# Kernel optimization log

Hardware: AMD Instinct MI355X
Metric: run time of the kernel (lower is better)

## Reference

```python
import jax, jax.numpy as jnp
import numpy as np

N_NODES = 16384
N_EDGES = 131072
MUL = 64                # multiplicity of 0e and 1o node irreps
N_RADIAL = 8
HIDDEN = 64
NUM_IRREPS = 6 * MUL    # 192x0e + 192x1o after concat/regroup
AVG_NUM_NEIGHBORS = 8.0
INV_SQRT3 = 1.0 / np.sqrt(3.0)  # wigner-3j(1,1,0) component normalization


def setup_inputs() -> dict:
    key = jax.random.key(0)
    ks = jax.random.split(key, 8)
    return {
        "node_feats": jax.random.normal(ks[0], (N_NODES, MUL + 3 * MUL), jnp.float32),
        "edge_features": jax.random.normal(ks[1], (N_EDGES, 4), jnp.float32),
        "radial_embedding": jax.random.uniform(ks[2], (N_EDGES, N_RADIAL), jnp.float32),
        "w1": jax.random.normal(ks[3], (N_RADIAL, HIDDEN), jnp.float32),
        "w2": jax.random.normal(ks[4], (HIDDEN, HIDDEN), jnp.float32),
        "w3": jax.random.normal(ks[5], (HIDDEN, NUM_IRREPS), jnp.float32),
        "senders": jax.random.randint(ks[6], (N_EDGES,), 0, N_NODES),
        "receivers": jax.random.randint(ks[7], (N_EDGES,), 0, N_NODES),
    }


def reference(node_feats, edge_features, radial_embedding, w1, w2, w3, senders, receivers):
    N = node_feats.shape[0]
    E = senders.shape[0]
    # split node irreps: 64x0e (scalars) + 64x1o (vectors)
    s = node_feats[:, :MUL]                       # [N, 64]
    v = node_feats[:, MUL:].reshape(N, MUL, 3)    # [N, 64, 3]
    # gather by sender
    s_e = s[senders]                              # [E, 64]
    v_e = v[senders]                              # [E, 64, 3]
    # edge attrs: 1x0e + 1x1o (spherical harmonics l<=1)
    es = edge_features[:, :1]                     # [E, 1]
    ev = edge_features[:, 1:4]                    # [E, 3]
    # CG tensor product filtered to {0e, 1o} (component normalization)
    tp_s1 = s_e * es                                              # 0e x 0e -> 0e
    tp_s2 = jnp.einsum("emc,ec->em", v_e, ev) * INV_SQRT3        # 1o x 1o -> 0e
    tp_v1 = s_e[:, :, None] * ev[:, None, :]                      # 0e x 1o -> 1o
    tp_v2 = v_e * es[:, :, None]                                  # 1o x 0e -> 1o
    # concat(filtered node feats, tp output) regrouped -> 192x0e + 192x1o
    scal = jnp.concatenate([s_e, tp_s1, tp_s2], axis=1)          # [E, 192]
    vec = jnp.concatenate([v_e, tp_v1, tp_v2], axis=1)           # [E, 192, 3]
    # radial MLP (no bias, e3nn 1/sqrt(fan_in) scaling, no output activation)
    h = jax.nn.silu(radial_embedding @ w1 / np.sqrt(N_RADIAL))
    h = jax.nn.silu(h @ w2 / np.sqrt(HIDDEN))
    w = h @ w3 / np.sqrt(HIDDEN)                                  # [E, 384]
    n_scal = scal.shape[1]
    scal = scal * w[:, :n_scal]
    vec = vec * w[:, n_scal:, None]
    # scatter-add into receivers
    out_s = jnp.zeros((N, n_scal), scal.dtype).at[receivers].add(scal)
    out_v = jnp.zeros((N, n_scal, 3), vec.dtype).at[receivers].add(vec)
    out = jnp.concatenate([out_s, out_v.reshape(N, n_scal * 3)], axis=1)
    return out / np.sqrt(AVG_NUM_NEIGHBORS)
```

## Files before the change

kernel.cpp:

```cpp
#include <hip/hip_runtime.h>

#define N_NODES 16384
#define N_EDGES 131072
#define MUL 64
#define HIDDEN 64
#define NUM_IRREPS 384
#define TE 64

#define INV_SQRT3   0.5773502691896258f
#define INV_SQRT8   0.35355339059327373f
#define SC3         (0.125f * 0.35355339059327373f)

typedef __attribute__((ext_vector_type(8))) __bf16 bf16x8;
typedef __attribute__((ext_vector_type(8))) unsigned short ushort8;
typedef __attribute__((ext_vector_type(4))) float f32x4;

union FragU { ushort8 u; bf16x8 b; };

__device__ __forceinline__ float silu_f(float x) {
    return x / (1.0f + __expf(-x));
}
__device__ __forceinline__ unsigned short bf16_rn(float f) {
    union { float f; unsigned int u; } c; c.f = f;
    unsigned int u = c.u + 0x7FFFu + ((c.u >> 16) & 1u);
    return (unsigned short)(u >> 16);
}
__device__ __forceinline__ float bf16_to_f(unsigned short h) {
    union { unsigned int u; float f; } c; c.u = ((unsigned int)h) << 16;
    return c.f;
}

__global__ __launch_bounds__(256) void pack_kernel(
    const float* __restrict__ w2, const float* __restrict__ w3,
    unsigned short* __restrict__ w2p, unsigned short* __restrict__ w3p)
{
    int t = blockIdx.x * 256 + threadIdx.x;
    float v;
    unsigned short *hi_dst, *lo_dst;
    if (t < 4096) {
        int K = t >> 11, T = (t >> 9) & 3, lane = (t >> 3) & 63, j = t & 7;
        int k = K * 32 + (lane >> 4) * 8 + j;
        int n = T * 16 + (lane & 15);
        v = w2[k * 64 + n] * 0.125f;
        hi_dst = w2p + t; lo_dst = w2p + 4096 + t;
    } else if (t < 28672) {
        int u = t - 4096;
        int K = u / 12288; int rem = u - K * 12288;
        int T = rem >> 9, lane = (rem >> 3) & 63, j = rem & 7;
        int k = K * 32 + (lane >> 4) * 8 + j;
        int n = T * 16 + (lane & 15);
        v = w3[k * 384 + n] * SC3;
        hi_dst = w3p + u; lo_dst = w3p + 24576 + u;
    } else {
        return;
    }
    unsigned short h = bf16_rn(v);
    unsigned short l = bf16_rn(v - bf16_to_f(h));
    *hi_dst = h; *lo_dst = l;
}

__global__ __launch_bounds__(256) void mlp_kernel(
    const float* __restrict__ radial,
    const float* __restrict__ w1,
    const unsigned short* __restrict__ w2p,
    const unsigned short* __restrict__ w3p,
    float* __restrict__ wout,
    int e_begin)
{
    __shared__ float w1s[512];
    __shared__ float rs[64 * 9];
    __shared__ float h1s[64 * 68];
    __shared__ float h2s[64 * 68];

    const int t   = threadIdx.x;
    const int le0 = blockIdx.x * TE;
    const int e0  = e_begin + le0;

    for (int i = t; i < 512; i += 256) w1s[i] = w1[i];
    for (int i = t; i < 512; i += 256)
        rs[(i >> 3) * 9 + (i & 7)] = radial[(size_t)e0 * 8 + i];
    __syncthreads();

    {
        const int e  = t >> 2;
        const int j0 = (t & 3) * 16;
        float acc[16];
#pragma unroll
        for (int j = 0; j < 16; ++j) acc[j] = 0.0f;
#pragma unroll
        for (int k = 0; k < 8; ++k) {
            float rv = rs[e * 9 + k];
#pragma unroll
            for (int j = 0; j < 16; ++j)
                acc[j] += rv * w1s[k * 64 + j0 + j];
        }
#pragma unroll
        for (int j = 0; j < 16; ++j)
            h1s[e * 68 + j0 + j] = silu_f(acc[j] * INV_SQRT8);
    }
    __syncthreads();

    const int lane = t & 63;
    const int wv   = t >> 6;
    const int m0   = wv * 16;
    const int quad = lane >> 4;
    const int l15  = lane & 15;

    FragU ah[2], al[2];

#pragma unroll
    for (int K = 0; K < 2; ++K) {
        const float4* p = (const float4*)&h1s[(m0 + l15) * 68 + K * 32 + quad * 8];
        float4 x0 = p[0], x1 = p[1];
        float xs[8] = {x0.x, x0.y, x0.z, x0.w, x1.x, x1.y, x1.z, x1.w};
#pragma unroll
        for (int j = 0; j < 8; ++j) {
            unsigned short h = bf16_rn(xs[j]);
            ah[K].u[j] = h;
            al[K].u[j] = bf16_rn(xs[j] - bf16_to_f(h));
        }
    }

#pragma unroll
    for (int T = 0; T < 4; ++T) {
        FragU bh0, bh1, bl0, bl1;
        bh0.u = *(const ushort8*)(w2p +        T * 512 + lane * 8);
        bh1.u = *(const ushort8*)(w2p + 2048 + T * 512 + lane * 8);
        bl0.u = *(const ushort8*)(w2p + 4096 + T * 512 + lane * 8);
        bl1.u = *(const ushort8*)(w2p + 6144 + T * 512 + lane * 8);
        f32x4 acc = {0.f, 0.f, 0.f, 0.f};
        acc = __builtin_amdgcn_mfma_f32_16x16x32_bf16(ah[0].b, bh0.b, acc, 0, 0, 0);
        acc = __builtin_amdgcn_mfma_f32_16x16x32_bf16(ah[1].b, bh1.b, acc, 0, 0, 0);
        acc = __builtin_amdgcn_mfma_f32_16x16x32_bf16(ah[0].b, bl0.b, acc, 0, 0, 0);
        acc = __builtin_amdgcn_mfma_f32_16x16x32_bf16(ah[1].b, bl1.b, acc, 0, 0, 0);
        acc = __builtin_amdgcn_mfma_f32_16x16x32_bf16(al[0].b, bh0.b, acc, 0, 0, 0);
        acc = __builtin_amdgcn_mfma_f32_16x16x32_bf16(al[1].b, bh1.b, acc, 0, 0, 0);
#pragma unroll
        for (int r = 0; r < 4; ++r)
            h2s[(m0 + quad * 4 + r) * 68 + T * 16 + l15] = silu_f(acc[r]);
    }
    __syncthreads();

#pragma unroll
    for (int K = 0; K < 2; ++K) {
        const float4* p = (const float4*)&h2s[(m0 + l15) * 68 + K * 32 + quad * 8];
        float4 x0 = p[0], x1 = p[1];
        float xs[8] = {x0.x, x0.y, x0.z, x0.w, x1.x, x1.y, x1.z, x1.w};
#pragma unroll
        for (int j = 0; j < 8; ++j) {
            unsigned short h = bf16_rn(xs[j]);
            ah[K].u[j] = h;
            al[K].u[j] = bf16_rn(xs[j] - bf16_to_f(h));
        }
    }

    for (int T = 0; T < 24; ++T) {
        FragU bh0, bh1, bl0, bl1;
        bh0.u = *(const ushort8*)(w3p +         T * 512 + lane * 8);
        bh1.u = *(const ushort8*)(w3p + 12288 + T * 512 + lane * 8);
        bl0.u = *(const ushort8*)(w3p + 24576 + T * 512 + lane * 8);
        bl1.u = *(const ushort8*)(w3p + 36864 + T * 512 + lane * 8);
        f32x4 acc = {0.f, 0.f, 0.f, 0.f};
        acc = __builtin_amdgcn_mfma_f32_16x16x32_bf16(ah[0].b, bh0.b, acc, 0, 0, 0);
        acc = __builtin_amdgcn_mfma_f32_16x16x32_bf16(ah[1].b, bh1.b, acc, 0, 0, 0);
        acc = __builtin_amdgcn_mfma_f32_16x16x32_bf16(ah[0].b, bl0.b, acc, 0, 0, 0);
        acc = __builtin_amdgcn_mfma_f32_16x16x32_bf16(ah[1].b, bl1.b, acc, 0, 0, 0);
        acc = __builtin_amdgcn_mfma_f32_16x16x32_bf16(al[0].b, bh0.b, acc, 0, 0, 0);
        acc = __builtin_amdgcn_mfma_f32_16x16x32_bf16(al[1].b, bh1.b, acc, 0, 0, 0);
#pragma unroll
        for (int r = 0; r < 4; ++r)
            wout[(size_t)(le0 + m0 + quad * 4 + r) * 384 + T * 16 + l15] = acc[r];
    }
}

__global__ __launch_bounds__(256) void hist_kernel(
    const int* __restrict__ receivers, int* __restrict__ counts)
{
    int e = blockIdx.x * 256 + threadIdx.x;
    if (e < N_EDGES) atomicAdd(&counts[receivers[e]], 1);
}

__global__ __launch_bounds__(256) void scan_kernel(
    const int* __restrict__ counts, int* __restrict__ offsets,
    int* __restrict__ cursor)
{
    __shared__ int sums[256];
    __shared__ int excl[256];
    const int t = threadIdx.x;
    const int base = t * 64;
    int s = 0;
    for (int i = 0; i < 64; ++i) s += counts[base + i];
    sums[t] = s;
    __syncthreads();
    if (t == 0) {
        int r = 0;
        for (int i = 0; i < 256; ++i) { excl[i] = r; r += sums[i]; }
    }
    __syncthreads();
    int run = excl[t];
    for (int i = 0; i < 64; ++i) {
        offsets[base + i] = run;
        cursor[base + i]  = run;
        run += counts[base + i];
    }
    if (t == 255) offsets[N_NODES] = run;
}

__global__ __launch_bounds__(256) void fill_kernel(
    const int* __restrict__ receivers, int* __restrict__ cursor,
    int* __restrict__ sorted)
{
    int e = blockIdx.x * 256 + threadIdx.x;
    if (e < N_EDGES) {
        int pos = atomicAdd(&cursor[receivers[e]], 1);
        sorted[pos] = e;
    }
}

__global__ __launch_bounds__(256) void accum_kernel(
    const float* __restrict__ node_feats,
    const float* __restrict__ edge_features,
    const float* __restrict__ wbuf,
    const int* __restrict__ senders,
    const int* __restrict__ sorted,
    const int* __restrict__ offsets,
    float* __restrict__ out,
    int e0, int cnt)
{
    const int n    = blockIdx.x;
    const int wid  = threadIdx.x >> 6;
    const int lane = threadIdx.x & 63;
    const int beg  = offsets[n];
    const int end  = offsets[n + 1];

    float as0 = 0.f, as1 = 0.f, as2 = 0.f;
    float av[3][3] = {};

    for (int i = beg + wid; i < end; i += 4) {
        const int e = sorted[i];
        if (e < e0 || e >= e0 + cnt) continue;

        const int sidx  = senders[e];
        const float es  = edge_features[e * 4 + 0];
        const float ev0 = edge_features[e * 4 + 1];
        const float ev1 = edge_features[e * 4 + 2];
        const float ev2 = edge_features[e * 4 + 3];

        const float* nf = node_feats + (size_t)sidx * 256;
        const float s  = nf[lane];
        const float v0 = nf[64 + lane * 3 + 0];
        const float v1 = nf[64 + lane * 3 + 1];
        const float v2 = nf[64 + lane * 3 + 2];

        const float* wp = wbuf + (size_t)(e - e0) * 384;
        const float ws0 = wp[lane];
        const float ws1 = wp[64 + lane];
        const float ws2 = wp[128 + lane];
        const float wv0 = wp[192 + lane];
        const float wv1 = wp[256 + lane];
        const float wv2 = wp[320 + lane];

        const float dot = (v0 * ev0 + v1 * ev1 + v2 * ev2) * INV_SQRT3;

        as0 += s * ws0;
        as1 += s * es * ws1;
        as2 += dot * ws2;

        av[0][0] += v0 * wv0; av[0][1] += v1 * wv0; av[0][2] += v2 * wv0;
        const float sw = s * wv1;
        av[1][0] += ev0 * sw; av[1][1] += ev1 * sw; av[1][2] += ev2 * sw;
        const float esw = es * wv2;
        av[2][0] += v0 * esw; av[2][1] += v1 * esw; av[2][2] += v2 * esw;
    }

    __shared__ float red[4 * 768];
    float* my = red + wid * 768;
    my[lane]        = as0;
    my[64 + lane]   = as1;
    my[128 + lane]  = as2;
#pragma unroll
    for (int c = 0; c < 3; ++c) {
        const int b = 192 + (c * 64 + lane) * 3;
        my[b + 0] = av[c][0];
        my[b + 1] = av[c][1];
        my[b + 2] = av[c][2];
    }
    __syncthreads();

    float* orow = out + (size_t)n * 768;
    for (int j = threadIdx.x; j < 768; j += 256) {
        float v = red[j] + red[768 + j] + red[1536 + j] + red[2304 + j];
        if (e0 == 0) orow[j] = v;
        else         orow[j] += v;
    }
}

extern "C" void kernel_launch(void* const* d_in, const int* in_sizes, int n_in,
                              void* d_out, int out_size, void* d_ws, size_t ws_size,
                              hipStream_t stream) {
    const float* node_feats    = (const float*)d_in[0];
    const float* edge_features = (const float*)d_in[1];
    const float* radial        = (const float*)d_in[2];
    const float* w1            = (const float*)d_in[3];
    const float* w2            = (const float*)d_in[4];
    const float* w3            = (const float*)d_in[5];
    const int*   senders       = (const int*)d_in[6];
    const int*   receivers     = (const int*)d_in[7];
    float* out = (float*)d_out;

    int* counts  = (int*)d_ws;
    int* offsets = counts + N_NODES;
    int* cursor  = offsets + N_NODES + 1;
    int* sorted  = cursor + N_NODES;
    size_t int_bytes = (size_t)((char*)(sorted + N_EDGES) - (char*)d_ws);
    size_t pk_off = (int_bytes + 255) & ~(size_t)255;
    unsigned short* w2p = (unsigned short*)((char*)d_ws + pk_off);
    unsigned short* w3p = w2p + 8192;
    size_t wbuf_off = (pk_off + (8192 + 49152) * sizeof(unsigned short) + 255) & ~(size_t)255;
    float* wbuf = (float*)((char*)d_ws + wbuf_off);

    hipMemsetAsync(counts, 0, (size_t)N_NODES * sizeof(int), stream);
    hist_kernel<<<(N_EDGES + 255) / 256, 256, 0, stream>>>(receivers, counts);
    scan_kernel<<<1, 256, 0, stream>>>(counts, offsets, cursor);
    fill_kernel<<<(N_EDGES + 255) / 256, 256, 0, stream>>>(receivers, cursor, sorted);
    pack_kernel<<<112, 256, 0, stream>>>(w2, w3, w2p, w3p);

    size_t avail = (ws_size > wbuf_off) ? (ws_size - wbuf_off) : 0;
    size_t max_chunk = avail / (NUM_IRREPS * sizeof(float));
    max_chunk &= ~(size_t)(TE - 1);
    int chunk = (max_chunk >= (size_t)N_EDGES) ? N_EDGES
              : (max_chunk < (size_t)TE ? TE : (int)max_chunk);

    for (int e0 = 0; e0 < N_EDGES; e0 += chunk) {
        int cnt = N_EDGES - e0;
        if (cnt > chunk) cnt = chunk;
        int nb1 = (cnt + TE - 1) / TE;
        mlp_kernel<<<nb1, 256, 0, stream>>>(radial, w1, w2p, w3p, wbuf, e0);
        accum_kernel<<<N_NODES, 256, 0, stream>>>(node_feats, edge_features, wbuf,
                                                  senders, sorted, offsets, out, e0, cnt);
    }
}
```

Measured before the change: 235.1 us.

## Store MLP edge weights as bf16 in receiver-sorted order for contiguous accumulation

The MLP kernel now processes edges in receiver-sorted order, gathering radial rows through the sorted index, and writes its 384 per-edge weights as bf16 instead of fp32. The accumulation kernel then reads the weight buffer contiguously by sorted position, not by scattered edge id. This halves the weight-buffer traffic and may allow larger chunks (possibly a single pass). The cost is precision loss from rounding the weights to bf16, plus a gathered radial load in the MLP.

```diff
diff --git a/kernel.cpp b/kernel.cpp
--- a/kernel.cpp
+++ b/kernel.cpp
@@ -2,8 +2,6 @@
 
 #define N_NODES 16384
 #define N_EDGES 131072
-#define MUL 64
-#define HIDDEN 64
 #define NUM_IRREPS 384
 #define TE 64
 
@@ -59,13 +57,58 @@
     *hi_dst = h; *lo_dst = l;
 }
 
+__global__ __launch_bounds__(256) void hist_kernel(
+    const int* __restrict__ receivers, int* __restrict__ counts)
+{
+    int e = blockIdx.x * 256 + threadIdx.x;
+    if (e < N_EDGES) atomicAdd(&counts[receivers[e]], 1);
+}
+
+__global__ __launch_bounds__(256) void scan_kernel(
+    const int* __restrict__ counts, int* __restrict__ offsets,
+    int* __restrict__ cursor)
+{
+    __shared__ int sums[256];
+    __shared__ int excl[256];
+    const int t = threadIdx.x;
+    const int base = t * 64;
+    int s = 0;
+    for (int i = 0; i < 64; ++i) s += counts[base + i];
+    sums[t] = s;
+    __syncthreads();
+    if (t == 0) {
+        int r = 0;
+        for (int i = 0; i < 256; ++i) { excl[i] = r; r += sums[i]; }
+    }
+    __syncthreads();
+    int run = excl[t];
+    for (int i = 0; i < 64; ++i) {
+        offsets[base + i] = run;
+        cursor[base + i]  = run;
+        run += counts[base + i];
+    }
+    if (t == 255) offsets[N_NODES] = run;
+}
+
+__global__ __launch_bounds__(256) void fill_kernel(
+    const int* __restrict__ receivers, int* __restrict__ cursor,
+    int* __restrict__ sorted)
+{
+    int e = blockIdx.x * 256 + threadIdx.x;
+    if (e < N_EDGES) {
+        int pos = atomicAdd(&cursor[receivers[e]], 1);
+        sorted[pos] = e;
+    }
+}
+
 __global__ __launch_bounds__(256) void mlp_kernel(
     const float* __restrict__ radial,
     const float* __restrict__ w1,
     const unsigned short* __restrict__ w2p,
     const unsigned short* __restrict__ w3p,
-    float* __restrict__ wout,
-    int e_begin)
+    const int* __restrict__ sorted,
+    unsigned short* __restrict__ wout,
+    int p_begin)
 {
     __shared__ float w1s[512];
     __shared__ float rs[64 * 9];
@@ -74,11 +117,16 @@
 
     const int t   = threadIdx.x;
     const int le0 = blockIdx.x * TE;
-    const int e0  = e_begin + le0;
+    const int p0  = p_begin + le0;
 
     for (int i = t; i < 512; i += 256) w1s[i] = w1[i];
-    for (int i = t; i < 512; i += 256)
-        rs[(i >> 3) * 9 + (i & 7)] = radial[(size_t)e0 * 8 + i];
+    if (t < 128) {
+        int j = t >> 1, half = t & 1;
+        int eid = sorted[p0 + j];
+        float4 rv = *(const float4*)&radial[(size_t)eid * 8 + half * 4];
+        float* d = &rs[j * 9 + half * 4];
+        d[0] = rv.x; d[1] = rv.y; d[2] = rv.z; d[3] = rv.w;
+    }
     __syncthreads();
 
     {
@@ -169,63 +217,19 @@
         acc = __builtin_amdgcn_mfma_f32_16x16x32_bf16(al[1].b, bh1.b, acc, 0, 0, 0);
 #pragma unroll
         for (int r = 0; r < 4; ++r)
-            wout[(size_t)(le0 + m0 + quad * 4 + r) * 384 + T * 16 + l15] = acc[r];
-    }
-}
-
-__global__ __launch_bounds__(256) void hist_kernel(
-    const int* __restrict__ receivers, int* __restrict__ counts)
-{
-    int e = blockIdx.x * 256 + threadIdx.x;
-    if (e < N_EDGES) atomicAdd(&counts[receivers[e]], 1);
-}
-
-__global__ __launch_bounds__(256) void scan_kernel(
-    const int* __restrict__ counts, int* __restrict__ offsets,
-    int* __restrict__ cursor)
-{
-    __shared__ int sums[256];
-    __shared__ int excl[256];
-    const int t = threadIdx.x;
-    const int base = t * 64;
-    int s = 0;
-    for (int i = 0; i < 64; ++i) s += counts[base + i];
-    sums[t] = s;
-    __syncthreads();
-    if (t == 0) {
-        int r = 0;
-        for (int i = 0; i < 256; ++i) { excl[i] = r; r += sums[i]; }
-    }
-    __syncthreads();
-    int run = excl[t];
-    for (int i = 0; i < 64; ++i) {
-        offsets[base + i] = run;
-        cursor[base + i]  = run;
-        run += counts[base + i];
-    }
-    if (t == 255) offsets[N_NODES] = run;
-}
-
-__global__ __launch_bounds__(256) void fill_kernel(
-    const int* __restrict__ receivers, int* __restrict__ cursor,
-    int* __restrict__ sorted)
-{
-    int e = blockIdx.x * 256 + threadIdx.x;
-    if (e < N_EDGES) {
-        int pos = atomicAdd(&cursor[receivers[e]], 1);
-        sorted[pos] = e;
+            wout[(size_t)(le0 + m0 + quad * 4 + r) * 384 + T * 16 + l15] = bf16_rn(acc[r]);
     }
 }
 
 __global__ __launch_bounds__(256) void accum_kernel(
     const float* __restrict__ node_feats,
     const float* __restrict__ edge_features,
-    const float* __restrict__ wbuf,
+    const unsigned short* __restrict__ wbuf,
     const int* __restrict__ senders,
     const int* __restrict__ sorted,
     const int* __restrict__ offsets,
     float* __restrict__ out,
-    int e0, int cnt)
+    int p0, int cnt)
 {
     const int n    = blockIdx.x;
     const int wid  = threadIdx.x >> 6;
@@ -237,9 +241,9 @@
     float av[3][3] = {};
 
     for (int i = beg + wid; i < end; i += 4) {
-        const int e = sorted[i];
-        if (e < e0 || e >= e0 + cnt) continue;
-
+        if (i < p0 || i >= p0 + cnt) continue;
+
+        const int e     = sorted[i];
         const int sidx  = senders[e];
         const float es  = edge_features[e * 4 + 0];
         const float ev0 = edge_features[e * 4 + 1];
@@ -252,13 +256,13 @@
         const float v1 = nf[64 + lane * 3 + 1];
         const float v2 = nf[64 + lane * 3 + 2];
 
-        const float* wp = wbuf + (size_t)(e - e0) * 384;
-        const float ws0 = wp[lane];
-        const float ws1 = wp[64 + lane];
-        const float ws2 = wp[128 + lane];
-        const float wv0 = wp[192 + lane];
-        const float wv1 = wp[256 + lane];
-        const float wv2 = wp[320 + lane];
+        const unsigned short* wp = wbuf + (size_t)(i - p0) * 384;
+        const float ws0 = bf16_to_f(wp[lane]);
+        const float ws1 = bf16_to_f(wp[64 + lane]);
+        const float ws2 = bf16_to_f(wp[128 + lane]);
+        const float wv0 = bf16_to_f(wp[192 + lane]);
+        const float wv1 = bf16_to_f(wp[256 + lane]);
+        const float wv2 = bf16_to_f(wp[320 + lane]);
 
         const float dot = (v0 * ev0 + v1 * ev1 + v2 * ev2) * INV_SQRT3;
 
@@ -290,7 +294,7 @@
     float* orow = out + (size_t)n * 768;
     for (int j = threadIdx.x; j < 768; j += 256) {
         float v = red[j] + red[768 + j] + red[1536 + j] + red[2304 + j];
-        if (e0 == 0) orow[j] = v;
+        if (p0 == 0) orow[j] = v;
         else         orow[j] += v;
     }
 }
@@ -317,26 +321,26 @@
     unsigned short* w2p = (unsigned short*)((char*)d_ws + pk_off);
     unsigned short* w3p = w2p + 8192;
     size_t wbuf_off = (pk_off + (8192 + 49152) * sizeof(unsigned short) + 255) & ~(size_t)255;
-    float* wbuf = (float*)((char*)d_ws + wbuf_off);
+    unsigned short* wbuf = (unsigned short*)((char*)d_ws + wbuf_off);
 
     hipMemsetAsync(counts, 0, (size_t)N_NODES * sizeof(int), stream);
     hist_kernel<<<(N_EDGES + 255) / 256, 256, 0, stream>>>(receivers, counts);
+    pack_kernel<<<112, 256, 0, stream>>>(w2, w3, w2p, w3p);
     scan_kernel<<<1, 256, 0, stream>>>(counts, offsets, cursor);
     fill_kernel<<<(N_EDGES + 255) / 256, 256, 0, stream>>>(receivers, cursor, sorted);
-    pack_kernel<<<112, 256, 0, stream>>>(w2, w3, w2p, w3p);
 
     size_t avail = (ws_size > wbuf_off) ? (ws_size - wbuf_off) : 0;
-    size_t max_chunk = avail / (NUM_IRREPS * sizeof(float));
+    size_t max_chunk = avail / (NUM_IRREPS * sizeof(unsigned short));
     max_chunk &= ~(size_t)(TE - 1);
     int chunk = (max_chunk >= (size_t)N_EDGES) ? N_EDGES
               : (max_chunk < (size_t)TE ? TE : (int)max_chunk);
 
-    for (int e0 = 0; e0 < N_EDGES; e0 += chunk) {
-        int cnt = N_EDGES - e0;
+    for (int p0 = 0; p0 < N_EDGES; p0 += chunk) {
+        int cnt = N_EDGES - p0;
         if (cnt > chunk) cnt = chunk;
         int nb1 = (cnt + TE - 1) / TE;
-        mlp_kernel<<<nb1, 256, 0, stream>>>(radial, w1, w2p, w3p, wbuf, e0);
+        mlp_kernel<<<nb1, 256, 0, stream>>>(radial, w1, w2p, w3p, sorted, wbuf, p0);
         accum_kernel<<<N_NODES, 256, 0, stream>>>(node_feats, edge_features, wbuf,
-                                                  senders, sorted, offsets, out, e0, cnt);
-    }
-}
+                                                  senders, sorted, offsets, out, p0, cnt);
+    }
+}
```

New measurement: 202.6 us. -13.8%, faster.
